# Kernel tuning notes

Measured on AMD Instinct MI355X. Metric: run time of the kernel, lower is better.

The kernel has to match this reference:

```python
import jax, jax.numpy as jnp
import numpy as np

B, S, E, H = 8, 1024, 1024, 16  # batch, seq, embed, heads; head_dim = E//H = 64

def setup_inputs() -> dict:
    key = jax.random.key(0)
    k1, k2, k3 = jax.random.split(key, 3)
    x = jax.random.normal(k1, (B, S, E), dtype=jnp.float32)
    W_attn = jax.random.normal(k2, (E, 3 * E), dtype=jnp.float32) * (1.0 / np.sqrt(E))
    W_proj = jax.random.normal(k3, (E, E), dtype=jnp.float32) * (1.0 / np.sqrt(E))
    return {"x": x, "W_attn": W_attn, "W_proj": W_proj}

def reference(x, W_attn, W_proj):
    b, s, e = x.shape
    d = e // H
    qkv = x @ W_attn                      # [b, s, 3e]
    q, k, v = jnp.split(qkv, 3, axis=-1)
    q = q.reshape(b, s, H, d)
    k = k.reshape(b, s, H, d)
    v = v.reshape(b, s, H, d)
    scale = 1.0 / np.sqrt(d).astype(np.float32)
    scores = jnp.einsum('bqhd,bkhd->bhqk', q, k) * scale  # [b, H, s, s]
    causal = jnp.tril(jnp.ones((s, s), dtype=bool))
    scores = jnp.where(causal[None, None, :, :], scores, -jnp.inf)
    attn = jax.nn.softmax(scores, axis=-1)
    y = jnp.einsum('bhqk,bkhd->bqhd', attn, v).reshape(b, s, e)
    return y @ W_proj
```

## Files before the change

### kernel.cpp

```cpp
#include <hip/hip_runtime.h>
#include <hip/hip_bf16.h>

typedef unsigned short u16;
typedef __attribute__((ext_vector_type(8))) short short8;
typedef __attribute__((ext_vector_type(4))) float f32x4;
typedef __attribute__((ext_vector_type(16))) float f32x16;
typedef __attribute__((ext_vector_type(4))) unsigned short u16x4;

#define DEVINL __device__ __forceinline__

DEVINL u16 f2bf(float f) {
    union { float f; unsigned u; } x; x.f = f;
    unsigned u = x.u;
    u += 0x7fffu + ((u >> 16) & 1u);
    return (u16)(u >> 16);
}

DEVINL void gload_lds16(const void* g, void* l) {
    __builtin_amdgcn_global_load_lds(
        (const __attribute__((address_space(1))) unsigned*)g,
        (__attribute__((address_space(3))) unsigned*)l, 16, 0, 0);
}

DEVINL int swz(int row) { return (((row & 7) ^ ((row >> 3) & 7)) << 4); }

DEVINL void swap32(unsigned& a, unsigned& b) {
#if __has_builtin(__builtin_amdgcn_permlane32_swap)
    typedef __attribute__((ext_vector_type(2))) unsigned uv2;
    uv2 r = __builtin_amdgcn_permlane32_swap(a, b, false, false);
    a = r.x; b = r.y;
#else
    int h = ((int)(threadIdx.x & 63)) >> 5;
    unsigned pa = (unsigned)__shfl_xor((int)a, 32);
    unsigned pb = (unsigned)__shfl_xor((int)b, 32);
    unsigned na = h ? pb : a;
    unsigned nb = h ? b : pa;
    a = na; b = nb;
#endif
}

__global__ void k_conv_x(const float* __restrict__ in, u16* __restrict__ out, int n4) {
    int i = blockIdx.x * blockDim.x + threadIdx.x;
    int stride = gridDim.x * blockDim.x;
    for (; i < n4; i += stride) {
        float4 v = ((const float4*)in)[i];
        u16x4 o;
        o.x = f2bf(v.x); o.y = f2bf(v.y); o.z = f2bf(v.z); o.w = f2bf(v.w);
        ((u16x4*)out)[i] = o;
    }
}

__global__ void k_transpose_bf(const float* __restrict__ in, u16* __restrict__ out, int R, int C) {
    __shared__ float t[32][33];
    int c0 = blockIdx.x * 32, r0 = blockIdx.y * 32;
    int tx = threadIdx.x, ty = threadIdx.y;
    #pragma unroll
    for (int j = 0; j < 32; j += 8)
        t[ty + j][tx] = in[(size_t)(r0 + ty + j) * C + c0 + tx];
    __syncthreads();
    #pragma unroll
    for (int j = 0; j < 32; j += 8)
        out[(size_t)(c0 + ty + j) * R + r0 + tx] = f2bf(t[tx][ty + j]);
}

template<int BM, int BN, bool OUT_BF16>
__global__ __launch_bounds__(512, 2)
void k_gemm_p(const u16* __restrict__ A, const u16* __restrict__ BT,
              void* __restrict__ C, int N, int K) {
    constexpr int BK = 32;
    constexpr int AI = BM / 128;
    constexpr int BI = BN / 128;
    constexpr int LOADS = AI + BI;
    constexpr int MF = BM / 2 / 16;
    constexpr int NF = BN / 4 / 16;
    constexpr int ABYTES = BM * BK * 2;
    constexpr int BBYTES = BN * BK * 2;
    constexpr int TBYTES = ABYTES + BBYTES;
    __shared__ char lds[3 * TBYTES];

    const int tid  = threadIdx.x;
    const int lane = tid & 63;
    const int lo   = lane & 15;
    const int hi   = lane >> 4;
    const int wave = tid >> 6;
    const int wm   = wave >> 2;
    const int wn   = wave & 3;

    const int gx   = gridDim.x;
    const int nwg  = gx * gridDim.y;
    const int orig = blockIdx.y * gx + blockIdx.x;
    const int wg   = (orig & 7) * (nwg >> 3) + (orig >> 3);
    const long row0 = (long)(wg / gx) * BM;
    const long col0 = (long)(wg % gx) * BN;

    f32x4 acc[MF][NF] = {};

    const int r0s = tid >> 2;
    const int sl  = tid & 3;

    const int NT = K >> 5;

    auto stage = [&](int t) {
        char* base = lds + (t % 3) * TBYTES;
        const int kb = t * BK;
        #pragma unroll
        for (int i = 0; i < AI; i++) {
            int r  = i * 128 + r0s;
            int kc = sl ^ (r & 3);
            gload_lds16(A + (row0 + r) * (size_t)K + kb + kc * 8,
                        base + i * 8192 + tid * 16);
        }
        #pragma unroll
        for (int i = 0; i < BI; i++) {
            int r  = i * 128 + r0s;
            int kc = sl ^ (r & 3);
            gload_lds16(BT + (col0 + r) * (size_t)K + kb + kc * 8,
                        base + ABYTES + i * 8192 + tid * 16);
        }
    };

    stage(0);
    stage(1);

    for (int t = 0; t < NT; t++) {
        if (t + 1 < NT) {
            if constexpr (LOADS == 4) asm volatile("s_waitcnt vmcnt(4)" ::: "memory");
            else                      asm volatile("s_waitcnt vmcnt(3)" ::: "memory");
        } else {
            asm volatile("s_waitcnt vmcnt(0)" ::: "memory");
        }
        __builtin_amdgcn_s_barrier();
        __builtin_amdgcn_sched_barrier(0);

        if (t + 2 < NT) stage(t + 2);

        const char* ab = lds + (t % 3) * TBYTES;
        const char* bb = ab + ABYTES;

        short8 af[MF], bfr[NF];
        #pragma unroll
        for (int m = 0; m < MF; m++) {
            int r = wm * (BM / 2) + m * 16 + lo;
            af[m] = *(const short8*)(ab + r * 64 + ((hi * 16) ^ ((r & 3) << 4)));
        }
        #pragma unroll
        for (int n = 0; n < NF; n++) {
            int r = wn * (BN / 4) + n * 16 + lo;
            bfr[n] = *(const short8*)(bb + r * 64 + ((hi * 16) ^ ((r & 3) << 4)));
        }

        __builtin_amdgcn_s_setprio(1);
        #pragma unroll
        for (int m = 0; m < MF; m++)
            #pragma unroll
            for (int n = 0; n < NF; n++)
                acc[m][n] = __builtin_amdgcn_mfma_f32_16x16x32_bf16(af[m], bfr[n], acc[m][n], 0, 0, 0);
        __builtin_amdgcn_s_setprio(0);
    }

    const int rl = hi * 4;
    #pragma unroll
    for (int m = 0; m < MF; m++)
        #pragma unroll
        for (int n = 0; n < NF; n++)
            #pragma unroll
            for (int r = 0; r < 4; r++) {
                long row = row0 + wm * (BM / 2) + m * 16 + rl + r;
                long col = col0 + wn * (BN / 4) + n * 16 + lo;
                if constexpr (OUT_BF16)
                    ((u16*)C)[row * (size_t)N + col] = f2bf(acc[m][n][r]);
                else
                    ((float*)C)[row * (size_t)N + col] = acc[m][n][r];
            }
}

#define SCALE_L2E 0.18033688011112042f

__global__ __launch_bounds__(256, 2)
void k_attn(const u16* __restrict__ qkv, u16* __restrict__ y) {
    constexpr int S = 1024, E = 1024, TE = 3072;
    __shared__ u16 Kt[64 * 64];
    __shared__ u16 Vt[64 * 64];

    const int tid  = threadIdx.x;
    const int lane = tid & 63;
    const int l31  = lane & 31;
    const int hA   = lane >> 5;
    const int wave = tid >> 6;

    const int qi = 7 - (int)(blockIdx.x >> 7);
    const int bh = blockIdx.x & 127;
    const int b  = bh >> 4;
    const int h  = bh & 15;
    const int q0 = qi * 128;
    const size_t rowbase = (size_t)b * S;
    const int qg = q0 + wave * 32 + l31;

    short8 qf[4];
    {
        const u16* qp = qkv + (rowbase + qg) * TE + h * 64 + hA * 8;
        #pragma unroll
        for (int kd = 0; kd < 4; kd++) qf[kd] = *(const short8*)(qp + kd * 16);
    }

    f32x16 o0 = {}, o1 = {};
    float ms = -1e30f, lsum = 0.f;

    const int kr0 = (wave << 3) + (lane >> 3);
    const int kcb = (lane & 7) * 16;
    const int vkv = (tid >> 3) * 2;
    const int vdc = (tid & 7) * 8;

    const int ntiles = 2 * qi + 2;
    for (int t = 0; t < ntiles; ++t) {
        const int kv0 = t * 64;
        __syncthreads();
        #pragma unroll
        for (int it = 0; it < 2; it++) {
            int r = kr0 + it * 32;
            const char* src = (const char*)qkv
                + (((rowbase + kv0 + r) * TE + E + h * 64) << 1) + (kcb ^ swz(r));
            gload_lds16(src, (char*)Kt + wave * 1024 + it * 4096);
        }
        {
            const u16* vsrc = qkv + (rowbase + kv0 + vkv) * TE + 2 * E + h * 64 + vdc;
            short8 v0 = *(const short8*)vsrc;
            short8 v1 = *(const short8*)(vsrc + TE);
            #pragma unroll
            for (int j = 0; j < 8; j++) {
                int d = vdc + j;
                unsigned val = (unsigned)(u16)v0[j] | ((unsigned)(u16)v1[j] << 16);
                *(unsigned*)((char*)Vt + d * 128 + ((vkv * 2) ^ swz(d))) = val;
            }
        }
        __syncthreads();

        const bool active = (kv0 <= q0 + wave * 32 + 31);
        if (!active) continue;

        f32x16 s0 = {}, s1 = {};
        #pragma unroll
        for (int kd = 0; kd < 4; kd++) {
            int r0 = l31, r1 = 32 + l31;
            short8 ka0 = *(const short8*)((const char*)Kt + r0 * 128 + ((kd * 32 + hA * 16) ^ swz(r0)));
            short8 ka1 = *(const short8*)((const char*)Kt + r1 * 128 + ((kd * 32 + hA * 16) ^ swz(r1)));
            s0 = __builtin_amdgcn_mfma_f32_32x32x16_bf16(ka0, qf[kd], s0, 0, 0, 0);
            s1 = __builtin_amdgcn_mfma_f32_32x32x16_bf16(ka1, qf[kd], s1, 0, 0, 0);
        }

        if (kv0 + 63 > q0 + wave * 32) {
            #pragma unroll
            for (int r = 0; r < 16; r++) {
                int kvr = kv0 + ((r & 3) + 8 * (r >> 2) + 4 * hA);
                if (kvr > qg)      s0[r] = -1e30f;
                if (kvr + 32 > qg) s1[r] = -1e30f;
            }
        }

        float pm = s0[0];
        #pragma unroll
        for (int r = 1; r < 16; r++) pm = fmaxf(pm, s0[r]);
        #pragma unroll
        for (int r = 0; r < 16; r++) pm = fmaxf(pm, s1[r]);
        pm = fmaxf(pm, __shfl_xor(pm, 32));
        float pms = pm * SCALE_L2E;
        if (__any(pms - ms > 8.0f)) {
            float msn = fmaxf(ms, pms);
            float alpha = exp2f(ms - msn);
            ms = msn;
            lsum *= alpha;
            #pragma unroll
            for (int r = 0; r < 16; r++) { o0[r] *= alpha; o1[r] *= alpha; }
        }

        float part = 0.f;
        #pragma unroll
        for (int r = 0; r < 16; r++) {
            float p0 = exp2f(s0[r] * SCALE_L2E - ms);
            float p1 = exp2f(s1[r] * SCALE_L2E - ms);
            s0[r] = p0; s1[r] = p1;
            part += p0 + p1;
        }
        lsum += part + __shfl_xor(part, 32);

        unsigned w0[8], w1[8];
        #pragma unroll
        for (int j = 0; j < 8; j++) {
            asm("v_cvt_pk_bf16_f32 %0, %1, %2" : "=v"(w0[j]) : "v"(s0[2 * j]), "v"(s0[2 * j + 1]));
            asm("v_cvt_pk_bf16_f32 %0, %1, %2" : "=v"(w1[j]) : "v"(s1[2 * j]), "v"(s1[2 * j + 1]));
        }

        #define PV_TILE(W, ST)                                                              \
        {                                                                                   \
            _Pragma("unroll")                                                               \
            for (int kkl = 0; kkl < 2; kkl++) {                                             \
                unsigned a  = W[4 * kkl],     bsw = W[4 * kkl + 2];                         \
                unsigned a2 = W[4 * kkl + 1], b2  = W[4 * kkl + 3];                         \
                swap32(a, bsw); swap32(a2, b2);                                             \
                union { int4 i; short8 s; } u;                                              \
                u.i = make_int4((int)a, (int)a2, (int)bsw, (int)b2);                        \
                {                                                                           \
                    int row = l31;                                                          \
                    short8 va = *(const short8*)((const char*)Vt + row * 128                \
                                  + (((ST) * 64 + kkl * 32 + hA * 16) ^ swz(row)));         \
                    o0 = __builtin_amdgcn_mfma_f32_32x32x16_bf16(va, u.s, o0, 0, 0, 0);     \
                }                                                                           \
                {                                                                           \
                    int row = 32 + l31;                                                     \
                    short8 va = *(const short8*)((const char*)Vt + row * 128                \
                                  + (((ST) * 64 + kkl * 32 + hA * 16) ^ swz(row)));         \
                    o1 = __builtin_amdgcn_mfma_f32_32x32x16_bf16(va, u.s, o1, 0, 0, 0);     \
                }                                                                           \
            }                                                                               \
        }
        PV_TILE(w0, 0)
        PV_TILE(w1, 1)
        #undef PV_TILE
    }

    __syncthreads();
    float rinv = 1.0f / lsum;
    u16* Ot = (wave < 2 ? Kt : Vt) + (wave & 1) * 2048;
    const int X = (l31 & 7) << 4;
    #pragma unroll
    for (int rq = 0; rq < 4; rq++) {
        u16x4 pk0, pk1;
        #pragma unroll
        for (int j = 0; j < 4; j++) {
            pk0[j] = f2bf(o0[4 * rq + j] * rinv);
            pk1[j] = f2bf(o1[4 * rq + j] * rinv);
        }
        *(u16x4*)((char*)Ot + l31 * 128 + ((16 * rq + 8 * hA) ^ X))      = pk0;
        *(u16x4*)((char*)Ot + l31 * 128 + ((64 + 16 * rq + 8 * hA) ^ X)) = pk1;
    }
    __syncthreads();
    #pragma unroll
    for (int p = 0; p < 4; p++) {
        int row = p * 8 + (lane >> 3);
        int cc  = lane & 7;
        short8 vv = *(const short8*)((const char*)Ot + row * 128
                      + ((cc * 16) ^ ((row & 7) << 4)));
        *(short8*)(y + (rowbase + q0 + wave * 32 + row) * E + h * 64 + cc * 8) = vv;
    }
}

extern "C" void kernel_launch(void* const* d_in, const int* in_sizes, int n_in,
                              void* d_out, int out_size, void* d_ws, size_t ws_size,
                              hipStream_t stream) {
    const float* x     = (const float*)d_in[0];
    const float* Wattn = (const float*)d_in[1];
    const float* Wproj = (const float*)d_in[2];
    float* out = (float*)d_out;

    char* ws = (char*)d_ws;
    u16* buf0 = (u16*)ws;
    u16* wT   = (u16*)(ws + 16777216);
    u16* qkv  = (u16*)(ws + 16777216 + 6291456);

    k_conv_x<<<2048, 256, 0, stream>>>(x, buf0, 8388608 / 4);
    k_transpose_bf<<<dim3(3072 / 32, 1024 / 32), dim3(32, 8), 0, stream>>>(Wattn, wT, 1024, 3072);
    k_gemm_p<256, 256, true><<<dim3(3072 / 256, 8192 / 256), 512, 0, stream>>>(buf0, wT, qkv, 3072, 1024);
    k_transpose_bf<<<dim3(1024 / 32, 1024 / 32), dim3(32, 8), 0, stream>>>(Wproj, wT, 1024, 1024);
    k_attn<<<dim3(1024), 256, 0, stream>>>(qkv, buf0);
    k_gemm_p<128, 256, false><<<dim3(1024 / 256, 8192 / 128), 512, 0, stream>>>(buf0, wT, out, 1024, 1024);
}
```

Measured before the change: 151.4 us.

## Rewrite GEMM as BK=64 double-buffered kernel with interleaved quarter-tile loads

Replaces the triple-buffered BK=32 GEMM with a BK=64 double-buffered kernel that uses an XOR swizzle over 8 chunks. Each K step is split into four MFMA phases, and global-to-LDS loads of the next tiles are spread between the phases. Fragment loads are also split across the phases. The goal is to hide memory latency behind MFMA work and cut per-iteration barrier overhead. In exchange it adds more barriers per iteration and more complex vmcnt accounting, which is fragile.

Result: faster. 146.2 us (-3.4%).

```diff
diff --git a/kernel.cpp b/kernel.cpp
--- a/kernel.cpp
+++ b/kernel.cpp
@@ -63,20 +63,34 @@
         out[(size_t)(c0 + ty + j) * R + r0 + tx] = f2bf(t[tx][ty + j]);
 }
 
+#define DO_MFMA(H, J)                                                            \
+    __builtin_amdgcn_s_barrier();                                                \
+    asm volatile("s_waitcnt lgkmcnt(0)" ::: "memory");                           \
+    __builtin_amdgcn_sched_barrier(0);                                           \
+    __builtin_amdgcn_s_setprio(1);                                               \
+    _Pragma("unroll")                                                            \
+    for (int m = 0; m < MFh; m++)                                                \
+        _Pragma("unroll")                                                        \
+        for (int n = 0; n < NFh; n++)                                            \
+            _Pragma("unroll")                                                    \
+            for (int kk = 0; kk < 2; kk++)                                       \
+                acc[(H) * MFh + m][(J) * NFh + n] =                              \
+                    __builtin_amdgcn_mfma_f32_16x16x32_bf16(                     \
+                        afr[m][kk], bfr[(J) * NFh + n][kk],                      \
+                        acc[(H) * MFh + m][(J) * NFh + n], 0, 0, 0);             \
+    __builtin_amdgcn_s_setprio(0);
+
 template<int BM, int BN, bool OUT_BF16>
 __global__ __launch_bounds__(512, 2)
-void k_gemm_p(const u16* __restrict__ A, const u16* __restrict__ BT,
-              void* __restrict__ C, int N, int K) {
-    constexpr int BK = 32;
-    constexpr int AI = BM / 128;
-    constexpr int BI = BN / 128;
-    constexpr int LOADS = AI + BI;
-    constexpr int MF = BM / 2 / 16;
-    constexpr int NF = BN / 4 / 16;
-    constexpr int ABYTES = BM * BK * 2;
-    constexpr int BBYTES = BN * BK * 2;
-    constexpr int TBYTES = ABYTES + BBYTES;
-    __shared__ char lds[3 * TBYTES];
+void k_gemm8(const u16* __restrict__ A, const u16* __restrict__ BT,
+             void* __restrict__ C, int N, int K) {
+    constexpr int MF  = BM / 32;
+    constexpr int NF  = BN / 64;
+    constexpr int MFh = MF / 2;
+    constexpr int NFh = NF / 2;
+    constexpr int ACH = BM / 64;
+    constexpr int TB  = (ACH + 4) * 8192;
+    __shared__ char lds[2 * TB];
 
     const int tid  = threadIdx.x;
     const int lane = tid & 63;
@@ -93,80 +107,101 @@
     const long row0 = (long)(wg / gx) * BM;
     const long col0 = (long)(wg % gx) * BN;
 
+    const int NT = K >> 6;
+
+    const int srow = tid >> 3;
+    const int gsb  = ((tid & 7) ^ (srow & 7)) << 4;
+
+    auto stA = [&](int c, int t) {
+        gload_lds16((const char*)(A + (row0 + c * 64 + srow) * (size_t)K + t * 64) + gsb,
+                    lds + (t & 1) * TB + c * 8192 + tid * 16);
+    };
+    auto stB = [&](int c, int t) {
+        gload_lds16((const char*)(BT + (col0 + c * 64 + srow) * (size_t)K + t * 64) + gsb,
+                    lds + (t & 1) * TB + (ACH + c) * 8192 + tid * 16);
+    };
+
     f32x4 acc[MF][NF] = {};
-
-    const int r0s = tid >> 2;
-    const int sl  = tid & 3;
-
-    const int NT = K >> 5;
-
-    auto stage = [&](int t) {
-        char* base = lds + (t % 3) * TBYTES;
-        const int kb = t * BK;
-        #pragma unroll
-        for (int i = 0; i < AI; i++) {
-            int r  = i * 128 + r0s;
-            int kc = sl ^ (r & 3);
-            gload_lds16(A + (row0 + r) * (size_t)K + kb + kc * 8,
-                        base + i * 8192 + tid * 16);
-        }
-        #pragma unroll
-        for (int i = 0; i < BI; i++) {
-            int r  = i * 128 + r0s;
-            int kc = sl ^ (r & 3);
-            gload_lds16(BT + (col0 + r) * (size_t)K + kb + kc * 8,
-                        base + ABYTES + i * 8192 + tid * 16);
-        }
-    };
-
-    stage(0);
-    stage(1);
+    short8 afr[MFh][2], bfr[NF][2];
+
+    const int xsw  = (lo & 7) << 4;
+    const int aRow = wm * (BM / 2) + lo;
+    const int bRow = wn * 64 + lo;
+
+    #pragma unroll
+    for (int c = 0; c < ACH; c++) stA(c, 0);
+    #pragma unroll
+    for (int c = 0; c < 4; c++) stB(c, 0);
+    #pragma unroll
+    for (int c = 0; c < ACH; c++) stA(c, 1);
+    stB(0, 1); stB(1, 1);
+    if constexpr (ACH == 4) asm volatile("s_waitcnt vmcnt(6)" ::: "memory");
+    else                    asm volatile("s_waitcnt vmcnt(4)" ::: "memory");
+    __builtin_amdgcn_s_barrier();
 
     for (int t = 0; t < NT; t++) {
-        if (t + 1 < NT) {
-            if constexpr (LOADS == 4) asm volatile("s_waitcnt vmcnt(4)" ::: "memory");
-            else                      asm volatile("s_waitcnt vmcnt(3)" ::: "memory");
+        const char* ab = lds + (t & 1) * TB;
+        const char* bb = ab + ACH * 8192;
+
+        #pragma unroll
+        for (int m = 0; m < MFh; m++) {
+            int r = aRow + m * 16;
+            #pragma unroll
+            for (int kk = 0; kk < 2; kk++)
+                afr[m][kk] = *(const short8*)(ab + r * 128 + ((kk * 64 + hi * 16) ^ xsw));
+        }
+        #pragma unroll
+        for (int n = 0; n < NFh; n++) {
+            int r = bRow + n * 16;
+            #pragma unroll
+            for (int kk = 0; kk < 2; kk++)
+                bfr[n][kk] = *(const short8*)(bb + r * 128 + ((kk * 64 + hi * 16) ^ xsw));
+        }
+        if (t + 1 < NT) { stB(2, t + 1); stB(3, t + 1); }
+        DO_MFMA(0, 0)
+        __builtin_amdgcn_s_barrier();
+
+        #pragma unroll
+        for (int n = NFh; n < NF; n++) {
+            int r = bRow + n * 16;
+            #pragma unroll
+            for (int kk = 0; kk < 2; kk++)
+                bfr[n][kk] = *(const short8*)(bb + r * 128 + ((kk * 64 + hi * 16) ^ xsw));
+        }
+        if (t + 2 < NT) { stB(0, t + 2); stB(1, t + 2); }
+        DO_MFMA(0, 1)
+        __builtin_amdgcn_s_barrier();
+
+        #pragma unroll
+        for (int m = 0; m < MFh; m++) {
+            int r = aRow + (MFh + m) * 16;
+            #pragma unroll
+            for (int kk = 0; kk < 2; kk++)
+                afr[m][kk] = *(const short8*)(ab + r * 128 + ((kk * 64 + hi * 16) ^ xsw));
+        }
+        if (t + 2 < NT) { stA(0, t + 2); if constexpr (ACH == 4) stA(2, t + 2); }
+        DO_MFMA(1, 0)
+        __builtin_amdgcn_s_barrier();
+
+        if (t + 2 < NT) { stA(1, t + 2); if constexpr (ACH == 4) stA(3, t + 2); }
+        DO_MFMA(1, 1)
+        if (t + 2 < NT) {
+            if constexpr (ACH == 4) asm volatile("s_waitcnt vmcnt(6)" ::: "memory");
+            else                    asm volatile("s_waitcnt vmcnt(4)" ::: "memory");
         } else {
             asm volatile("s_waitcnt vmcnt(0)" ::: "memory");
         }
         __builtin_amdgcn_s_barrier();
-        __builtin_amdgcn_sched_barrier(0);
-
-        if (t + 2 < NT) stage(t + 2);
-
-        const char* ab = lds + (t % 3) * TBYTES;
-        const char* bb = ab + ABYTES;
-
-        short8 af[MF], bfr[NF];
-        #pragma unroll
-        for (int m = 0; m < MF; m++) {
-            int r = wm * (BM / 2) + m * 16 + lo;
-            af[m] = *(const short8*)(ab + r * 64 + ((hi * 16) ^ ((r & 3) << 4)));
-        }
-        #pragma unroll
-        for (int n = 0; n < NF; n++) {
-            int r = wn * (BN / 4) + n * 16 + lo;
-            bfr[n] = *(const short8*)(bb + r * 64 + ((hi * 16) ^ ((r & 3) << 4)));
-        }
-
-        __builtin_amdgcn_s_setprio(1);
-        #pragma unroll
-        for (int m = 0; m < MF; m++)
-            #pragma unroll
-            for (int n = 0; n < NF; n++)
-                acc[m][n] = __builtin_amdgcn_mfma_f32_16x16x32_bf16(af[m], bfr[n], acc[m][n], 0, 0, 0);
-        __builtin_amdgcn_s_setprio(0);
-    }
-
-    const int rl = hi * 4;
+    }
+
     #pragma unroll
     for (int m = 0; m < MF; m++)
         #pragma unroll
         for (int n = 0; n < NF; n++)
             #pragma unroll
             for (int r = 0; r < 4; r++) {
-                long row = row0 + wm * (BM / 2) + m * 16 + rl + r;
-                long col = col0 + wn * (BN / 4) + n * 16 + lo;
+                long row = row0 + wm * (BM / 2) + m * 16 + hi * 4 + r;
+                long col = col0 + wn * 64 + n * 16 + lo;
                 if constexpr (OUT_BF16)
                     ((u16*)C)[row * (size_t)N + col] = f2bf(acc[m][n][r]);
                 else
@@ -359,8 +394,8 @@
 
     k_conv_x<<<2048, 256, 0, stream>>>(x, buf0, 8388608 / 4);
     k_transpose_bf<<<dim3(3072 / 32, 1024 / 32), dim3(32, 8), 0, stream>>>(Wattn, wT, 1024, 3072);
-    k_gemm_p<256, 256, true><<<dim3(3072 / 256, 8192 / 256), 512, 0, stream>>>(buf0, wT, qkv, 3072, 1024);
+    k_gemm8<256, 256, true><<<dim3(3072 / 256, 8192 / 256), 512, 0, stream>>>(buf0, wT, qkv, 3072, 1024);
     k_transpose_bf<<<dim3(1024 / 32, 1024 / 32), dim3(32, 8), 0, stream>>>(Wproj, wT, 1024, 1024);
     k_attn<<<dim3(1024), 256, 0, stream>>>(qkv, buf0);
-    k_gemm_p<128, 256, false><<<dim3(1024 / 256, 8192 / 128), 512, 0, stream>>>(buf0, wT, out, 1024, 1024);
-}
+    k_gemm8<128, 256, false><<<dim3(1024 / 256, 8192 / 128), 512, 0, stream>>>(buf0, wT, out, 1024, 1024);
+}
```
